# Kernel tuning notes

Measured on AMD Instinct MI355X. Metric: run time of the kernel, lower is better.

The kernel has to match this reference:

```python
import jax, jax.numpy as jnp
import numpy as np

B, L, D_IN, H, FEAT, PROJ = 1024, 128, 130, 768, 49, 40


def setup_inputs() -> dict:
    key = jax.random.key(0)
    ks = jax.random.split(key, 16)
    s = 0.05
    return {
        "X": jax.random.normal(ks[0], (B, L, D_IN), dtype=jnp.float32),
        "Fe": jax.random.normal(ks[1], (B, FEAT), dtype=jnp.float32),
        # three attention heads densa1/2/3 stacked: [3, H, L]
        "W_att": jax.random.normal(ks[2], (3, H, L), dtype=jnp.float32) * s,
        "b_att": jax.random.normal(ks[3], (3, L), dtype=jnp.float32) * s,
        # LSTMCell(3*D_IN, H) params, PyTorch layout
        "W_ih": jax.random.normal(ks[4], (4 * H, 3 * D_IN), dtype=jnp.float32) * s,
        "W_hh": jax.random.normal(ks[5], (4 * H, H), dtype=jnp.float32) * s,
        "b_ih": jax.random.normal(ks[6], (4 * H,), dtype=jnp.float32) * s,
        "b_hh": jax.random.normal(ks[7], (4 * H,), dtype=jnp.float32) * s,
        # Dense1: Linear(H, FEAT)
        "W_d1": jax.random.normal(ks[8], (FEAT, H), dtype=jnp.float32) * s,
        "b_d1": jax.random.normal(ks[9], (FEAT,), dtype=jnp.float32) * s,
        # AttFeat R: Linear(FEAT, PROJ); A: Linear(PROJ, 1, bias=False)
        "W_r": jax.random.normal(ks[10], (PROJ, FEAT), dtype=jnp.float32) * s,
        "b_r": jax.random.normal(ks[11], (PROJ,), dtype=jnp.float32) * s,
        "W_a": jax.random.normal(ks[12], (1, PROJ), dtype=jnp.float32) * s,
        # Dense2: Linear(PROJ, 2)
        "W_d2": jax.random.normal(ks[13], (2, PROJ), dtype=jnp.float32) * s,
        "b_d2": jax.random.normal(ks[14], (2,), dtype=jnp.float32) * s,
    }


def reference(X, Fe, W_att, b_att, W_ih, W_hh, b_ih, b_hh, W_d1, b_d1, W_r, b_r, W_a, W_d2, b_d2):
    b = X.shape[0]

    def step(carry, _):
        h, c = carry
        # three softmax attention distributions over the sequence: [b, 3, L]
        logits = jnp.einsum('bh,khl->bkl', h, W_att) + b_att
        alp = jax.nn.softmax(logits, axis=-1)
        # weighted sums over seq -> concat of v1,v2,v3: [b, 3*D_IN]
        v = jnp.einsum('bkl,bld->bkd', alp, X).reshape(b, -1)
        # PyTorch LSTMCell update
        gates = v @ W_ih.T + b_ih + h @ W_hh.T + b_hh
        i, f, g, o = jnp.split(gates, 4, axis=-1)
        c_new = jax.nn.sigmoid(f) * c + jax.nn.sigmoid(i) * jnp.tanh(g)
        h_new = jax.nn.sigmoid(o) * jnp.tanh(c_new)
        return (h_new, c_new), h_new

    h0 = jnp.zeros((b, H), dtype=X.dtype)
    c0 = jnp.zeros((b, H), dtype=X.dtype)
    _, hs = jax.lax.scan(step, (h0, c0), None, length=L)  # [L, b, H]
    out = jnp.transpose(hs, (1, 0, 2))                    # [b, L, H]

    # MaxLayer: max-pool over the sequence dim
    x = jnp.max(out, axis=1)                              # [b, H]

    # Dense1 + ReLU
    y = jax.nn.relu(x @ W_d1.T + b_d1)                    # [b, FEAT]

    # AttFeat over [y, Fe]
    r1 = jax.nn.leaky_relu(y @ W_r.T + b_r)               # [b, PROJ]
    r2 = jax.nn.leaky_relu(Fe @ W_r.T + b_r)
    a1 = jnp.tanh(r1) @ W_a.T                             # [b, 1]
    a2 = jnp.tanh(r2) @ W_a.T
    a = jax.nn.softmax(jnp.concatenate([a1, a2], axis=-1), axis=-1)  # [b, 2]
    s = jax.nn.relu(a[:, 0:1] * r1 + a[:, 1:2] * r2)      # [b, PROJ]

    # Dense2 (squeeze is a no-op for b > 1)
    return s @ W_d2.T + b_d2                              # [b, 2]
```

## Files before the change

kernel.cpp:

```cpp
#include <hip/hip_runtime.h>
#include <stdint.h>


#define B_SZ   1024
#define LSEQ   128
#define DIN    130
#define HDIM   768
#define NFEAT  49
#define NPROJ  40
#define KPAD   1216
#define VOFF   416
#define NGATE  3072
#define KT_G   19
#define XELEM  (LSEQ * DIN)
#define GBUF   24576

typedef unsigned short u16;
typedef __attribute__((ext_vector_type(8))) short short8;
typedef __attribute__((ext_vector_type(4))) float f32x4;

__device__ __forceinline__ u16 f2bf(float f) {
  unsigned int u = __float_as_uint(f);
  u += 0x7FFFu + ((u >> 16) & 1u);
  return (u16)(u >> 16);
}
__device__ __forceinline__ float bf2f(u16 b) {
  return __uint_as_float(((unsigned int)b) << 16);
}
__device__ __forceinline__ float frcp(float x) {
  return __builtin_amdgcn_rcpf(x);
}
__device__ __forceinline__ float ftanh(float x) {
  return 1.f - 2.f * frcp(1.f + __expf(2.f * x));
}
__device__ __forceinline__ float fsigm(float x) {
  return frcp(1.f + __expf(-x));
}
__device__ __forceinline__ void gload16(const void* g, void* l) {
  __builtin_amdgcn_global_load_lds(
      (__attribute__((address_space(1))) const void*)g,
      (__attribute__((address_space(3))) void*)l, 16, 0, 0);
}

__global__ __launch_bounds__(256, 4) void gemm_logits_k(
    const u16* __restrict__ Ah,
    const u16* __restrict__ Bh, float* __restrict__ Cp)
{
  __shared__ __align__(16) u16 sAh[32 * 40];
  __shared__ __align__(16) u16 sBh[64 * 40];

  const int tid = threadIdx.x, lane = tid & 63, wid = tid >> 6;
  const int wm = (wid & 1) * 16, wn = (wid >> 1) * 32;
  const int lm = lane & 15, quad = lane >> 4;
  const int bm = blockIdx.x * 32, bn = blockIdx.y * 64;
  const int kh = blockIdx.z;
  const int kbase = kh * 384;
  float* __restrict__ C = Cp + (size_t)kh * B_SZ * 384;

  const bool aload = tid < 128;
  const int ar = tid >> 2, ac = (tid & 3) * 8;
  const size_t a_off = (size_t)(bm + ar) * KPAD + kbase + ac;
  const size_t b_off = (size_t)(bn + ar) * HDIM + kbase + ac;

  uint4 ph, pb;
  if (aload) ph = *(const uint4*)(Ah + a_off);
  pb = *(const uint4*)(Bh + b_off);

  f32x4 acc0 = {0.f, 0.f, 0.f, 0.f}, acc1 = {0.f, 0.f, 0.f, 0.f};

  for (int kt = 0; kt < 12; ++kt) {
    if (aload) *(uint4*)&sAh[ar * 40 + ac] = ph;
    *(uint4*)&sBh[ar * 40 + ac] = pb;
    __syncthreads();
    if (kt + 1 < 12) {
      const int k0 = (kt + 1) * 32;
      if (aload) ph = *(const uint4*)(Ah + a_off + k0);
      pb = *(const uint4*)(Bh + b_off + k0);
    }
    const short8 ah = *(const short8*)&sAh[(wm + lm) * 40 + quad * 8];
    const short8 b0 = *(const short8*)&sBh[(wn + lm) * 40 + quad * 8];
    const short8 b1 = *(const short8*)&sBh[(wn + 16 + lm) * 40 + quad * 8];
    acc0 = __builtin_amdgcn_mfma_f32_16x16x32_bf16(ah, b0, acc0, 0, 0, 0);
    acc1 = __builtin_amdgcn_mfma_f32_16x16x32_bf16(ah, b1, acc1, 0, 0, 0);
    __syncthreads();
  }

  const int col = bn + wn + lm;
  const int row0 = bm + wm + quad * 4;
#pragma unroll
  for (int r = 0; r < 4; ++r) {
    C[(size_t)(row0 + r) * 384 + col]      = acc0[r];
    C[(size_t)(row0 + r) * 384 + col + 16] = acc1[r];
  }
}

__global__ __launch_bounds__(256, 2) void gates_lstm(
    const u16* __restrict__ Ah,
    const u16* __restrict__ Wh,
    const float* __restrict__ bsum,
    float* __restrict__ cst, float* __restrict__ hmax,
    u16* __restrict__ out_h)
{
  __shared__ __align__(16) char smem[2 * GBUF];

  const int tid = threadIdx.x, lane = tid & 63, wid = tid >> 6;
  const int wm = (wid >> 1) * 64, wn = (wid & 1) * 32;
  const int lm = lane & 15, quad = lane >> 4;

  const int wg = blockIdx.x;
  const int wid2 = (wg & 7) * 48 + (wg >> 3);
  const int bm = (wid2 & 7) * 128;
  const int j0 = (wid2 >> 3) * 16;

  const u16* Asrc[4];
#pragma unroll
  for (int i = 0; i < 4; ++i) {
    const int r = i * 32 + wid * 8 + (lane >> 3);
    const int s = (lane & 7) ^ (r & 7);
    Asrc[i] = Ah + (size_t)(bm + r) * KPAD + (s << 3);
  }
  const u16* Bsrc[2];
#pragma unroll
  for (int i = 0; i < 2; ++i) {
    const int r = i * 32 + wid * 8 + (lane >> 3);
    const int s = (lane & 7) ^ (r & 7);
    const int nrow = (r >> 4) * HDIM + j0 + (r & 15);
    Bsrc[i] = Wh + (size_t)nrow * KPAD + (s << 3);
  }

  int aoff[4], boff[2];
#pragma unroll
  for (int mi = 0; mi < 4; ++mi) {
    const int R = wm + mi * 16 + lm;
    aoff[mi] = R * 64 + ((quad ^ (R & 7)) << 3);
  }
#pragma unroll
  for (int ni = 0; ni < 2; ++ni) {
    const int R = wn + ni * 16 + lm;
    boff[ni] = R * 64 + ((quad ^ (R & 7)) << 3);
  }

  f32x4 acc[4][2];
#pragma unroll
  for (int mi = 0; mi < 4; ++mi)
#pragma unroll
    for (int ni = 0; ni < 2; ++ni) acc[mi][ni] = (f32x4){0.f, 0.f, 0.f, 0.f};

  auto stage = [&](int buf, int kt) {
    char* bb = smem + buf * GBUF;
    const int k0 = kt * 64;
#pragma unroll
    for (int i = 0; i < 4; ++i)
      gload16(Asrc[i] + k0, bb + ((i << 12) + (wid << 10)));
#pragma unroll
    for (int i = 0; i < 2; ++i)
      gload16(Bsrc[i] + k0, bb + 16384 + ((i << 12) + (wid << 10)));
  };

  stage(0, 0);
  __syncthreads();

  for (int kt = 0; kt < KT_G; ++kt) {
    if (kt + 1 < KT_G) stage((kt + 1) & 1, kt + 1);
    const u16* sA = (const u16*)(smem + (kt & 1) * GBUF);
    const u16* sB = sA + 8192;
#pragma unroll
    for (int kk = 0; kk < 2; ++kk) {
      const int kx = kk << 5;
      short8 af[4], bg[2];
#pragma unroll
      for (int mi = 0; mi < 4; ++mi)
        af[mi] = *(const short8*)(sA + (aoff[mi] ^ kx));
#pragma unroll
      for (int ni = 0; ni < 2; ++ni)
        bg[ni] = *(const short8*)(sB + (boff[ni] ^ kx));
#pragma unroll
      for (int mi = 0; mi < 4; ++mi)
#pragma unroll
        for (int ni = 0; ni < 2; ++ni)
          acc[mi][ni] = __builtin_amdgcn_mfma_f32_16x16x32_bf16(
              af[mi], bg[ni], acc[mi][ni], 0, 0, 0);
    }
    __syncthreads();
  }

  float* tile = (float*)smem;
#pragma unroll
  for (int mi = 0; mi < 4; ++mi)
#pragma unroll
    for (int ni = 0; ni < 2; ++ni) {
      const int c = wn + ni * 16 + lm;
#pragma unroll
      for (int r = 0; r < 4; ++r)
        tile[(wm + mi * 16 + quad * 4 + r) * 68 + c] = acc[mi][ni][r];
    }
  __syncthreads();

#pragma unroll
  for (int i = 0; i < 8; ++i) {
    const int lin = tid + 256 * i;
    const int row = lin >> 4, jj = lin & 15;
    const int b = bm + row, j = j0 + jj;
    const float* tr = tile + row * 68;
    const float pi = tr[jj]      + bsum[j];
    const float pf = tr[16 + jj] + bsum[HDIM + j];
    const float pg = tr[32 + jj] + bsum[2 * HDIM + j];
    const float po = tr[48 + jj] + bsum[3 * HDIM + j];
    const float si = fsigm(pi);
    const float sf = fsigm(pf);
    const float so = fsigm(po);
    const size_t cidx = (size_t)b * HDIM + j;
    const float cn = sf * cst[cidx] + si * ftanh(pg);
    const float hn = so * ftanh(cn);
    cst[cidx] = cn;
    hmax[cidx] = fmaxf(hmax[cidx], hn);
    out_h[(size_t)b * KPAD + VOFF + j] = f2bf(hn);
  }
}

__global__ __launch_bounds__(512, 4) void softmax_v(
    const float* __restrict__ l0, const float* __restrict__ l1,
    const float* __restrict__ b_att,
    const u16* __restrict__ XT,
    u16* __restrict__ act)
{
  const int b = blockIdx.x;
  const int t = threadIdx.x;
  __shared__ __align__(16) u16 sXT[XELEM];
  __shared__ __align__(16) float s_alp[384];
  __shared__ float s_w[16];

  {
    const uint4* src = (const uint4*)(XT + (size_t)b * XELEM);
    uint4* dst = (uint4*)sXT;
#pragma unroll
    for (int rep = 0; rep < 4; ++rep) {
      const int i = t + rep * 512;
      const int d = i >> 4, blk = i & 15;
      dst[d * 16 + (blk ^ (d & 7))] = src[i];
    }
    if (t < 32) {
      const int i = 2048 + t;
      const int d = i >> 4, blk = i & 15;
      dst[d * 16 + (blk ^ (d & 7))] = src[i];
    }
  }

  const int lane = t & 63, wv = t >> 6, hw = wv & ~1;
  float x = -3.4e38f;
  if (t < 384)
    x = l0[(size_t)b * 384 + t] + l1[(size_t)b * 384 + t] + b_att[t];

  float m = x;
#pragma unroll
  for (int off = 32; off > 0; off >>= 1) m = fmaxf(m, __shfl_xor(m, off));
  if (lane == 0 && wv < 6) s_w[wv] = m;
  __syncthreads();

  float e = 0.f;
  if (t < 384) e = __expf(x - fmaxf(s_w[hw], s_w[hw | 1]));
  float sum = e;
#pragma unroll
  for (int off = 32; off > 0; off >>= 1) sum += __shfl_xor(sum, off);
  if (lane == 0 && wv < 6) s_w[8 + wv] = sum;
  __syncthreads();

  if (t < 384) {
    const float sk = s_w[8 + hw] + s_w[8 + (hw | 1)];
    s_alp[t] = e * frcp(sk);
  }
  __syncthreads();

  if (t < 390) {
    const int k = t / 130;
    const int d = t - k * 130;
    const uint4* xr = (const uint4*)sXT;
    const int dbase = d * 16, dsw = d & 7;
    const float* ab = s_alp + (k << 7);
    float acc = 0.f;
#pragma unroll
    for (int c = 0; c < 16; ++c) {
      const uint4 raw = xr[dbase + (c ^ dsw)];
      const float4 a0 = *(const float4*)(ab + (c << 3));
      const float4 a1 = *(const float4*)(ab + (c << 3) + 4);
      acc += a0.x * bf2f((u16)(raw.x & 0xffff));
      acc += a0.y * bf2f((u16)(raw.x >> 16));
      acc += a0.z * bf2f((u16)(raw.y & 0xffff));
      acc += a0.w * bf2f((u16)(raw.y >> 16));
      acc += a1.x * bf2f((u16)(raw.z & 0xffff));
      acc += a1.y * bf2f((u16)(raw.z >> 16));
      acc += a1.z * bf2f((u16)(raw.w & 0xffff));
      acc += a1.w * bf2f((u16)(raw.w >> 16));
    }
    act[(size_t)b * KPAD + t] = f2bf(acc);
  }
}

__global__ __launch_bounds__(64) void final_head(
    const float* __restrict__ hmax, const float* __restrict__ Fe,
    const float* __restrict__ W_d1, const float* __restrict__ b_d1,
    const float* __restrict__ W_r,  const float* __restrict__ b_r,
    const float* __restrict__ W_a,
    const float* __restrict__ W_d2, const float* __restrict__ b_d2,
    float* __restrict__ out)
{
  const int b = blockIdx.x;
  const int t = threadIdx.x;
  __shared__ float sx[HDIM];
  __shared__ float sy[NFEAT];
  __shared__ float sr1[NPROJ], sr2[NPROJ];
  __shared__ float sa[2];

  for (int i = t; i < HDIM; i += 64) sx[i] = hmax[(size_t)b * HDIM + i];
  __syncthreads();

  if (t < NFEAT) {
    float acc = b_d1[t];
    const float* w = W_d1 + (size_t)t * HDIM;
    for (int i = 0; i < HDIM; ++i) acc += sx[i] * w[i];
    sy[t] = fmaxf(acc, 0.f);
  }
  __syncthreads();

  if (t < NPROJ) {
    float a1 = b_r[t], a2 = b_r[t];
    const float* w  = W_r + (size_t)t * NFEAT;
    const float* fe = Fe + (size_t)b * NFEAT;
    for (int i = 0; i < NFEAT; ++i) { a1 += sy[i] * w[i]; a2 += fe[i] * w[i]; }
    sr1[t] = (a1 > 0.f) ? a1 : 0.01f * a1;
    sr2[t] = (a2 > 0.f) ? a2 : 0.01f * a2;
  }
  __syncthreads();

  if (t == 0) {
    float a1 = 0.f, a2 = 0.f;
    for (int p = 0; p < NPROJ; ++p) {
      a1 += tanhf(sr1[p]) * W_a[p];
      a2 += tanhf(sr2[p]) * W_a[p];
    }
    const float mx = fmaxf(a1, a2);
    const float e1 = expf(a1 - mx), e2 = expf(a2 - mx);
    sa[0] = e1 / (e1 + e2);
    sa[1] = e2 / (e1 + e2);
  }
  __syncthreads();

  if (t < 2) {
    float acc = b_d2[t];
    const float* w = W_d2 + (size_t)t * NPROJ;
    for (int p = 0; p < NPROJ; ++p) {
      float s = sa[0] * sr1[p] + sa[1] * sr2[p];
      s = fmaxf(s, 0.f);
      acc += s * w[p];
    }
    out[(size_t)b * 2 + t] = acc;
  }
}

__global__ __launch_bounds__(256) void pack_w(
    const float* __restrict__ W_ih, const float* __restrict__ W_hh,
    const float* __restrict__ b_ih, const float* __restrict__ b_hh,
    u16* __restrict__ hi, float* __restrict__ bsum)
{
  const int idx = blockIdx.x * 256 + threadIdx.x;
  if (idx >= NGATE * KPAD) return;
  const int n = idx / KPAD;
  const int k = idx - n * KPAD;
  float v = 0.f;
  if (k < 3 * DIN)                       v = W_ih[(size_t)n * (3 * DIN) + k];
  else if (k >= VOFF && k < VOFF + HDIM) v = W_hh[(size_t)n * HDIM + (k - VOFF)];
  hi[idx] = f2bf(v);
  if (k == 0) bsum[n] = b_ih[n] + b_hh[n];
}

__global__ __launch_bounds__(256) void pack_watt(
    const float* __restrict__ W_att,
    u16* __restrict__ hi)
{
  const int idx = blockIdx.x * 256 + threadIdx.x;
  if (idx >= 384 * HDIM) return;
  const int n = idx / HDIM;
  const int h = idx - n * HDIM;
  const int katt = n >> 7;
  const int l = n & 127;
  hi[idx] = f2bf(W_att[((size_t)katt * HDIM + h) * LSEQ + l]);
}

__global__ __launch_bounds__(256) void pack_xt(
    const float* __restrict__ X, u16* __restrict__ XT)
{
  const int b = blockIdx.x;
  const int t = threadIdx.x;
  __shared__ u16 sX[XELEM];
  const float* src = X + (size_t)b * XELEM;
  for (int i = t; i < XELEM; i += 256) sX[i] = f2bf(src[i]);
  __syncthreads();
  uint4* dst = (uint4*)(XT + (size_t)b * XELEM);
  for (int u = t; u < 2080; u += 256) {
    const int d = u >> 4, blk = u & 15;
    const int lb = blk * 8;
    ushort4 w0, w1;
    w0.x = sX[(lb + 0) * DIN + d]; w0.y = sX[(lb + 1) * DIN + d];
    w0.z = sX[(lb + 2) * DIN + d]; w0.w = sX[(lb + 3) * DIN + d];
    w1.x = sX[(lb + 4) * DIN + d]; w1.y = sX[(lb + 5) * DIN + d];
    w1.z = sX[(lb + 6) * DIN + d]; w1.w = sX[(lb + 7) * DIN + d];
    uint4 o;
    o.x = (unsigned)w0.x | ((unsigned)w0.y << 16);
    o.y = (unsigned)w0.z | ((unsigned)w0.w << 16);
    o.z = (unsigned)w1.x | ((unsigned)w1.y << 16);
    o.w = (unsigned)w1.z | ((unsigned)w1.w << 16);
    dst[u] = o;
  }
}

__global__ __launch_bounds__(256) void init_state(
    u16* __restrict__ a0, u16* __restrict__ a1,
    float* __restrict__ cst, float* __restrict__ hmax)
{
  const int idx = blockIdx.x * 256 + threadIdx.x;
  if (idx < B_SZ * KPAD) { a0[idx] = 0; a1[idx] = 0; }
  if (idx < B_SZ * HDIM) { cst[idx] = 0.f; hmax[idx] = -3.4e38f; }
}

extern "C" void kernel_launch(void* const* d_in, const int* in_sizes, int n_in,
                              void* d_out, int out_size, void* d_ws, size_t ws_size,
                              hipStream_t stream) {
  const float* X     = (const float*)d_in[0];
  const float* Fe    = (const float*)d_in[1];
  const float* W_att = (const float*)d_in[2];
  const float* b_att = (const float*)d_in[3];
  const float* W_ih  = (const float*)d_in[4];
  const float* W_hh  = (const float*)d_in[5];
  const float* b_ih  = (const float*)d_in[6];
  const float* b_hh  = (const float*)d_in[7];
  const float* W_d1  = (const float*)d_in[8];
  const float* b_d1  = (const float*)d_in[9];
  const float* W_r   = (const float*)d_in[10];
  const float* b_r   = (const float*)d_in[11];
  const float* W_a   = (const float*)d_in[12];
  const float* W_d2  = (const float*)d_in[13];
  const float* b_d2  = (const float*)d_in[14];
  float* out = (float*)d_out;

  char* base = (char*)d_ws;
  size_t off = 0;
  auto alloc = [&](size_t nbytes) -> void* {
    void* p = base + off;
    off = (off + nbytes + 255) & ~(size_t)255;
    return p;
  };
  u16* act0    = (u16*)alloc((size_t)B_SZ * KPAD * 2);
  u16* act1    = (u16*)alloc((size_t)B_SZ * KPAD * 2);
  u16* wcat    = (u16*)alloc((size_t)NGATE * KPAD * 2);
  u16* watt    = (u16*)alloc((size_t)384 * HDIM * 2);
  u16* xt16    = (u16*)alloc((size_t)B_SZ * XELEM * 2);
  float* bsum  = (float*)alloc((size_t)NGATE * 4);
  float* lpart = (float*)alloc((size_t)2 * B_SZ * 384 * 4);
  float* cst   = (float*)alloc((size_t)B_SZ * HDIM * 4);
  float* hmax  = (float*)alloc((size_t)B_SZ * HDIM * 4);

  pack_w<<<(NGATE * KPAD + 255) / 256, 256, 0, stream>>>(W_ih, W_hh, b_ih, b_hh, wcat, bsum);
  pack_watt<<<(384 * HDIM + 255) / 256, 256, 0, stream>>>(W_att, watt);
  pack_xt<<<B_SZ, 256, 0, stream>>>(X, xt16);
  init_state<<<(B_SZ * KPAD + 255) / 256, 256, 0, stream>>>(act0, act1, cst, hmax);

  float* l0 = lpart;
  float* l1 = lpart + (size_t)B_SZ * 384;

  gemm_logits_k<<<dim3(B_SZ / 32, 384 / 64, 2), 256, 0, stream>>>(act0 + VOFF, watt, lpart);
  softmax_v<<<B_SZ, 512, 0, stream>>>(l0, l1, b_att, xt16, act0);

  u16 *rd = act0, *wr = act1;
  for (int step = 0; step < LSEQ; ++step) {
    gates_lstm<<<dim3(384), 256, 0, stream>>>(rd, wcat, bsum, cst, hmax, wr);
    if (step + 1 < LSEQ) {
      gemm_logits_k<<<dim3(B_SZ / 32, 384 / 64, 2), 256, 0, stream>>>(wr + VOFF, watt, lpart);
      softmax_v<<<B_SZ, 512, 0, stream>>>(l0, l1, b_att, xt16, wr);
    }
    u16* tt = rd; rd = wr; wr = tt;
  }

  final_head<<<B_SZ, 64, 0, stream>>>(hmax, Fe, W_d1, b_d1, W_r, b_r, W_a, W_d2, b_d2, out);
}
```

Baseline: 4.495 ms.

## Retile LSTM gate GEMM to 64x96 tiles and read X directly in softmax_v

The gate GEMM tile changes from 128 rows x 16 hidden units (64 gate columns) to 64 rows x 24 hidden units (96 gate columns). The grid grows from 384 to 512 workgroups, which should fill the CUs better, and shared memory per block shrinks. The epilogue is adjusted to the new tile shape. Separately, softmax_v drops its 32KB shared-memory staging of the per-batch X slice and reads bf16 X straight from global memory, which removes LDS pressure and lets more blocks run per CU. The cost is uncoalesced strided global reads that depend on cache hits.

New measurement: 5.041 ms. 1.12x slower.

```diff
diff --git a/kernel.cpp b/kernel.cpp
--- a/kernel.cpp
+++ b/kernel.cpp
@@ -13,7 +13,7 @@
 #define NGATE  3072
 #define KT_G   19
 #define XELEM  (LSEQ * DIN)
-#define GBUF   24576
+#define GBUF   20480
 
 typedef unsigned short u16;
 typedef __attribute__((ext_vector_type(8))) short short8;
@@ -104,57 +104,57 @@
   __shared__ __align__(16) char smem[2 * GBUF];
 
   const int tid = threadIdx.x, lane = tid & 63, wid = tid >> 6;
-  const int wm = (wid >> 1) * 64, wn = (wid & 1) * 32;
+  const int wm = (wid >> 1) * 32, wn = (wid & 1) * 48;
   const int lm = lane & 15, quad = lane >> 4;
 
   const int wg = blockIdx.x;
-  const int wid2 = (wg & 7) * 48 + (wg >> 3);
-  const int bm = (wid2 & 7) * 128;
-  const int j0 = (wid2 >> 3) * 16;
-
-  const u16* Asrc[4];
-#pragma unroll
-  for (int i = 0; i < 4; ++i) {
+  const int vid = (wg & 7) * 64 + (wg >> 3);
+  const int bm = (vid & 15) * 64;
+  const int j0 = (vid >> 4) * 24;
+
+  const u16* Asrc[2];
+#pragma unroll
+  for (int i = 0; i < 2; ++i) {
     const int r = i * 32 + wid * 8 + (lane >> 3);
     const int s = (lane & 7) ^ (r & 7);
     Asrc[i] = Ah + (size_t)(bm + r) * KPAD + (s << 3);
   }
-  const u16* Bsrc[2];
-#pragma unroll
-  for (int i = 0; i < 2; ++i) {
+  const u16* Bsrc[3];
+#pragma unroll
+  for (int i = 0; i < 3; ++i) {
     const int r = i * 32 + wid * 8 + (lane >> 3);
     const int s = (lane & 7) ^ (r & 7);
-    const int nrow = (r >> 4) * HDIM + j0 + (r & 15);
+    const int nrow = (r / 24) * HDIM + j0 + (r % 24);
     Bsrc[i] = Wh + (size_t)nrow * KPAD + (s << 3);
   }
 
-  int aoff[4], boff[2];
-#pragma unroll
-  for (int mi = 0; mi < 4; ++mi) {
+  int aoff[2], boff[3];
+#pragma unroll
+  for (int mi = 0; mi < 2; ++mi) {
     const int R = wm + mi * 16 + lm;
     aoff[mi] = R * 64 + ((quad ^ (R & 7)) << 3);
   }
 #pragma unroll
-  for (int ni = 0; ni < 2; ++ni) {
+  for (int ni = 0; ni < 3; ++ni) {
     const int R = wn + ni * 16 + lm;
     boff[ni] = R * 64 + ((quad ^ (R & 7)) << 3);
   }
 
-  f32x4 acc[4][2];
-#pragma unroll
-  for (int mi = 0; mi < 4; ++mi)
-#pragma unroll
-    for (int ni = 0; ni < 2; ++ni) acc[mi][ni] = (f32x4){0.f, 0.f, 0.f, 0.f};
+  f32x4 acc[2][3];
+#pragma unroll
+  for (int mi = 0; mi < 2; ++mi)
+#pragma unroll
+    for (int ni = 0; ni < 3; ++ni) acc[mi][ni] = (f32x4){0.f, 0.f, 0.f, 0.f};
 
   auto stage = [&](int buf, int kt) {
     char* bb = smem + buf * GBUF;
     const int k0 = kt * 64;
 #pragma unroll
-    for (int i = 0; i < 4; ++i)
+    for (int i = 0; i < 2; ++i)
       gload16(Asrc[i] + k0, bb + ((i << 12) + (wid << 10)));
 #pragma unroll
-    for (int i = 0; i < 2; ++i)
-      gload16(Bsrc[i] + k0, bb + 16384 + ((i << 12) + (wid << 10)));
+    for (int i = 0; i < 3; ++i)
+      gload16(Bsrc[i] + k0, bb + 8192 + ((i << 12) + (wid << 10)));
   };
 
   stage(0, 0);
@@ -163,21 +163,21 @@
   for (int kt = 0; kt < KT_G; ++kt) {
     if (kt + 1 < KT_G) stage((kt + 1) & 1, kt + 1);
     const u16* sA = (const u16*)(smem + (kt & 1) * GBUF);
-    const u16* sB = sA + 8192;
+    const u16* sB = sA + 4096;
 #pragma unroll
     for (int kk = 0; kk < 2; ++kk) {
       const int kx = kk << 5;
-      short8 af[4], bg[2];
-#pragma unroll
-      for (int mi = 0; mi < 4; ++mi)
+      short8 af[2], bg[3];
+#pragma unroll
+      for (int mi = 0; mi < 2; ++mi)
         af[mi] = *(const short8*)(sA + (aoff[mi] ^ kx));
 #pragma unroll
-      for (int ni = 0; ni < 2; ++ni)
+      for (int ni = 0; ni < 3; ++ni)
         bg[ni] = *(const short8*)(sB + (boff[ni] ^ kx));
 #pragma unroll
-      for (int mi = 0; mi < 4; ++mi)
-#pragma unroll
-        for (int ni = 0; ni < 2; ++ni)
+      for (int mi = 0; mi < 2; ++mi)
+#pragma unroll
+        for (int ni = 0; ni < 3; ++ni)
           acc[mi][ni] = __builtin_amdgcn_mfma_f32_16x16x32_bf16(
               af[mi], bg[ni], acc[mi][ni], 0, 0, 0);
     }
@@ -186,26 +186,26 @@
 
   float* tile = (float*)smem;
 #pragma unroll
-  for (int mi = 0; mi < 4; ++mi)
-#pragma unroll
-    for (int ni = 0; ni < 2; ++ni) {
+  for (int mi = 0; mi < 2; ++mi)
+#pragma unroll
+    for (int ni = 0; ni < 3; ++ni) {
       const int c = wn + ni * 16 + lm;
 #pragma unroll
       for (int r = 0; r < 4; ++r)
-        tile[(wm + mi * 16 + quad * 4 + r) * 68 + c] = acc[mi][ni][r];
-    }
-  __syncthreads();
-
-#pragma unroll
-  for (int i = 0; i < 8; ++i) {
+        tile[(wm + mi * 16 + quad * 4 + r) * 100 + c] = acc[mi][ni][r];
+    }
+  __syncthreads();
+
+#pragma unroll
+  for (int i = 0; i < 6; ++i) {
     const int lin = tid + 256 * i;
-    const int row = lin >> 4, jj = lin & 15;
+    const int row = lin / 24, jj = lin - row * 24;
     const int b = bm + row, j = j0 + jj;
-    const float* tr = tile + row * 68;
+    const float* tr = tile + row * 100;
     const float pi = tr[jj]      + bsum[j];
-    const float pf = tr[16 + jj] + bsum[HDIM + j];
-    const float pg = tr[32 + jj] + bsum[2 * HDIM + j];
-    const float po = tr[48 + jj] + bsum[3 * HDIM + j];
+    const float pf = tr[24 + jj] + bsum[HDIM + j];
+    const float pg = tr[48 + jj] + bsum[2 * HDIM + j];
+    const float po = tr[72 + jj] + bsum[3 * HDIM + j];
     const float si = fsigm(pi);
     const float sf = fsigm(pf);
     const float so = fsigm(po);
@@ -226,25 +226,8 @@
 {
   const int b = blockIdx.x;
   const int t = threadIdx.x;
-  __shared__ __align__(16) u16 sXT[XELEM];
   __shared__ __align__(16) float s_alp[384];
   __shared__ float s_w[16];
-
-  {
-    const uint4* src = (const uint4*)(XT + (size_t)b * XELEM);
-    uint4* dst = (uint4*)sXT;
-#pragma unroll
-    for (int rep = 0; rep < 4; ++rep) {
-      const int i = t + rep * 512;
-      const int d = i >> 4, blk = i & 15;
-      dst[d * 16 + (blk ^ (d & 7))] = src[i];
-    }
-    if (t < 32) {
-      const int i = 2048 + t;
-      const int d = i >> 4, blk = i & 15;
-      dst[d * 16 + (blk ^ (d & 7))] = src[i];
-    }
-  }
 
   const int lane = t & 63, wv = t >> 6, hw = wv & ~1;
   float x = -3.4e38f;
@@ -274,13 +257,12 @@
   if (t < 390) {
     const int k = t / 130;
     const int d = t - k * 130;
-    const uint4* xr = (const uint4*)sXT;
-    const int dbase = d * 16, dsw = d & 7;
+    const uint4* xg = (const uint4*)(XT + (size_t)b * XELEM + (d << 7));
     const float* ab = s_alp + (k << 7);
     float acc = 0.f;
 #pragma unroll
     for (int c = 0; c < 16; ++c) {
-      const uint4 raw = xr[dbase + (c ^ dsw)];
+      const uint4 raw = xg[c];
       const float4 a0 = *(const float4*)(ab + (c << 3));
       const float4 a1 = *(const float4*)(ab + (c << 3) + 4);
       acc += a0.x * bf2f((u16)(raw.x & 0xffff));
@@ -472,7 +454,7 @@
 
   u16 *rd = act0, *wr = act1;
   for (int step = 0; step < LSEQ; ++step) {
-    gates_lstm<<<dim3(384), 256, 0, stream>>>(rd, wcat, bsum, cst, hmax, wr);
+    gates_lstm<<<dim3(512), 256, 0, stream>>>(rd, wcat, bsum, cst, hmax, wr);
     if (step + 1 < LSEQ) {
       gemm_logits_k<<<dim3(B_SZ / 32, 384 / 64, 2), 256, 0, stream>>>(wr + VOFF, watt, lpart);
       softmax_v<<<B_SZ, 512, 0, stream>>>(l0, l1, b_att, xt16, wr);
```
